# Kernel optimization log

Hardware: AMD Instinct MI355X
Metric: run time of the kernel (lower is better)

The kernel has to match this reference:

```python
import jax, jax.numpy as jnp
import numpy as np

M, K, N, R = 8192, 4096, 4096, 64  # tokens, in_features, out_features, pod_rank


def _unpack_int4(packed):
    """Unpack bytes (stored as int32 in [0,256)) into signed int4 values in [-8,7].
    Low nibble is element 2k, high nibble is element 2k+1."""
    b = packed.astype(jnp.int32)
    low = ((b & 0xF) ^ 8) - 8
    high = (((b >> 4) & 0xF) ^ 8) - 8
    out = jnp.stack([low, high], axis=-1)
    return out.reshape(packed.shape[:-1] + (packed.shape[-1] * 2,))


def setup_inputs() -> dict:
    key = jax.random.key(0)
    ks = jax.random.split(key, 7)
    x_quant = jax.random.randint(ks[0], (M, K // 2), 0, 256, dtype=jnp.int32)
    x_scale = jax.random.uniform(ks[1], (M,), dtype=jnp.float32) * 0.01 + 1e-4
    weight = jax.random.randint(ks[2], (N, K // 2), 0, 256, dtype=jnp.int32)
    weight_scales = jax.random.uniform(ks[3], (N, 1), dtype=jnp.float32) * 0.01 + 1e-4
    bias = jax.random.normal(ks[4], (N,), dtype=jnp.float32) * 0.02
    x_r = jax.random.normal(ks[5], (M, R), dtype=jnp.float32)
    w_outlier = jax.random.normal(ks[6], (N, R), dtype=jnp.float32) * 0.02
    return {"x_quant": x_quant, "x_scale": x_scale, "weight": weight,
            "weight_scales": weight_scales, "bias": bias, "x_r": x_r,
            "w_outlier": w_outlier}


def reference(x_quant, x_scale, weight, weight_scales, bias, x_r, w_outlier):
    xi = _unpack_int4(x_quant)          # [M, K] int32 in [-8,7]
    wi = _unpack_int4(weight)           # [N, K] int32 in [-8,7]
    y_int = jnp.matmul(xi, wi.T)        # [M, N] int32 accumulator
    # dequant: per-token activation scale * per-channel weight scale, plus bias
    y = (y_int.astype(jnp.float32) * x_scale[:, None] * weight_scales.reshape(1, -1)
         + bias[None, :])
    # fused low-rank outlier correction: addmm_(x_r, w_outlier.T)
    y = y + jnp.matmul(x_r, w_outlier.T)
    return y
```

## Files before the change

kernel.cpp:

```cpp
#include <hip/hip_runtime.h>
#include <hip/hip_fp16.h>

typedef int      v4i __attribute__((ext_vector_type(4)));
typedef int      v2i __attribute__((ext_vector_type(2)));
typedef float    v4f __attribute__((ext_vector_type(4)));
typedef _Float16 v8h __attribute__((ext_vector_type(8)));
typedef _Float16 v4h __attribute__((ext_vector_type(4)));

#define MDIM 8192
#define NDIM 4096
#define KDIM 4096
#define RDIM 64
#define KW   (KDIM / 2)
#define NT   (KDIM / 128)

typedef const __attribute__((address_space(1))) char* gas_ptr;
typedef __attribute__((address_space(3))) char*       las_ptr;

__device__ __forceinline__ void unpack_w(v4i w, int& lo8, int& hi8) {
    unsigned p01 = __builtin_amdgcn_perm((unsigned)w.y, (unsigned)w.x, 0x0C0C0400u);
    unsigned p23 = __builtin_amdgcn_perm((unsigned)w.w, (unsigned)w.z, 0x0C0C0400u);
    unsigned b4  = __builtin_amdgcn_perm(p23, p01, 0x05040100u);
    unsigned lo = b4 & 0x0F0F0F0Fu;
    unsigned hi = (b4 >> 4) & 0x0F0F0F0Fu;
    lo8 = (int)(((lo ^ 0x08080808u) + 0x78787878u) ^ 0x80808080u);
    hi8 = (int)(((hi ^ 0x08080808u) + 0x78787878u) ^ 0x80808080u);
}

__global__ __launch_bounds__(256)
void repack_int4(const int* __restrict__ xq, const int* __restrict__ wq,
                 char* __restrict__ x8, char* __restrict__ w8)
{
    const size_t XCH = (size_t)MDIM * KW / 4;
    const size_t TCH = XCH + (size_t)NDIM * KW / 4;
    size_t stride = (size_t)gridDim.x * blockDim.x;
    for (size_t i = (size_t)blockIdx.x * blockDim.x + threadIdx.x; i < TCH; i += stride) {
        const int* src;
        char* dst;
        if (i < XCH) { src = xq + i * 4; dst = x8 + i * 8; }
        else { size_t j = i - XCH; src = wq + j * 4; dst = w8 + j * 8; }
        v4i w = *(const v4i*)src;
        int lo8, hi8;
        unpack_w(w, lo8, hi8);
        *(v2i*)dst = (v2i){lo8, hi8};
    }
}

__device__ __forceinline__ void stage2(const char* g, char* l, int kt, int ks) {
    const char* s = g + kt * 128 + ks * 64;
    __builtin_amdgcn_global_load_lds((gas_ptr)(const void*)s,
                                     (las_ptr)(void*)l, 16, 0, 0);
    __builtin_amdgcn_global_load_lds((gas_ptr)(const void*)(s + (size_t)128 * KDIM),
                                     (las_ptr)(void*)(l + 8192), 16, 0, 0);
}

#define BAR asm volatile("s_barrier" ::: "memory")
#define VM4 asm volatile("s_waitcnt vmcnt(4)" ::: "memory")
#define SGB(m, n) __builtin_amdgcn_sched_group_barrier(m, n, 0)

#define SGBSEQ do {                                                            \
    SGB(0x100, 2); SGB(0x8, 4); SGB(0x100, 2); SGB(0x8, 4);                    \
    SGB(0x100, 2); SGB(0x8, 4); SGB(0x100, 2); SGB(0x8, 4);                    \
    SGB(0x100, 2); SGB(0x8, 4); SGB(0x100, 2); SGB(0x8, 4);                    \
    SGB(0x30, 2);  SGB(0x8, 4); SGB(0x30, 2);  SGB(0x8, 4);                    \
} while (0)

#define READ_A8(dst, PAR, KS)                                                  \
    _Pragma("unroll")                                                          \
    for (int ii = 0; ii < 8; ++ii)                                             \
        dst[ii] = *(const v4i*)((const char*)Asub[PAR][KS] + aoff + ii * 1024)

#define READ_B4(dst, PAR, KS)                                                  \
    _Pragma("unroll")                                                          \
    for (int jj = 0; jj < 4; ++jj)                                             \
        dst[jj] = *(const v4i*)((const char*)Bsub[PAR][KS] + boff + jj * 1024)

#define MMA32(AS, BS)                                                          \
    _Pragma("unroll")                                                          \
    for (int ii = 0; ii < 8; ++ii)                                             \
        _Pragma("unroll")                                                      \
        for (int jj = 0; jj < 4; ++jj)                                         \
            acc[ii][jj] = __builtin_amdgcn_mfma_i32_16x16x64_i8(               \
                AS[ii], BS[jj], acc[ii][jj], 0, 0, 0)

#define QPHASE(CA, CB, NA, NB, NPAR, NKS, SPAR, SKS, SKT) do {                 \
    READ_A8(NA, NPAR, NKS);                                                    \
    READ_B4(NB, NPAR, NKS);                                                    \
    stage2(gA, &Asub[SPAR][SKS][ldsW], SKT, SKS);                              \
    stage2(gB, &Bsub[SPAR][SKS][ldsW], SKT, SKS);                              \
    MMA32(CA, CB);                                                             \
    SGBSEQ;                                                                    \
    VM4; BAR;                                                                  \
} while (0)

__global__ __launch_bounds__(512, 2)
void w4a4_gemm8(const char* __restrict__ x8, const char* __restrict__ w8,
                const float* __restrict__ xsc, const float* __restrict__ wsc,
                const float* __restrict__ bias, const float* __restrict__ xr,
                const float* __restrict__ wo, float* __restrict__ out)
{
    __shared__ __align__(16) char Asub[2][2][16384];
    __shared__ __align__(16) char Bsub[2][2][16384];
    __shared__ float xs_s[256];
    __shared__ float ws_s[256];
    __shared__ float bs_s[256];

    const int tid  = threadIdx.x;
    const int lane = tid & 63;
    const int wid  = tid >> 6;
    const int wm   = wid >> 2;
    const int wn   = wid & 3;

    const int s  = (blockIdx.x & 7) * 64 + (blockIdx.x >> 3);
    const int by = s >> 4;
    const int bxn = s & 15;

    if (tid < 256) {
        xs_s[tid] = xsc[by * 256 + tid];
    } else {
        int n = tid - 256;
        ws_s[n] = wsc[bxn * 256 + n];
        bs_s[n] = bias[bxn * 256 + n];
    }

    const int srow = wid * 16 + (lane >> 2);
    const int scol = ((lane & 3) * 16) ^ (((lane >> 3) & 3) << 4);
    const char* gA = x8 + (size_t)(by * 256 + srow) * KDIM + scol;
    const char* gB = w8 + (size_t)(bxn * 256 + srow) * KDIM + scol;
    const int ldsW = wid * 1024;

    const int lr   = lane & 15;
    const int cef  = ((lane >> 4) << 4) ^ (((lr >> 1) & 3) << 4);
    const int aoff = (wm * 128 + lr) * 64 + cef;
    const int boff = (wn * 64  + lr) * 64 + cef;

    v4i acc[8][4];
#pragma unroll
    for (int i = 0; i < 8; ++i)
#pragma unroll
        for (int j = 0; j < 4; ++j) acc[i][j] = (v4i){0, 0, 0, 0};

    stage2(gA, &Asub[0][0][ldsW], 0, 0);
    stage2(gB, &Bsub[0][0][ldsW], 0, 0);
    stage2(gA, &Asub[0][1][ldsW], 0, 1);
    stage2(gB, &Bsub[0][1][ldsW], 0, 1);
    stage2(gA, &Asub[1][0][ldsW], 1, 0);
    stage2(gB, &Bsub[1][0][ldsW], 1, 0);
    VM4;
    BAR;

    v4i fa0[8], fb0[4], fa1[8], fb1[4];
    READ_A8(fa0, 0, 0);
    READ_B4(fb0, 0, 0);

    for (int it = 0; it < NT / 2; ++it) {
        const int kt1 = 2 * it + 1;
        const int kt2 = (2 * it + 2 < NT) ? 2 * it + 2 : NT - 1;
        const int kt3 = (2 * it + 3 < NT) ? 2 * it + 3 : NT - 1;
        QPHASE(fa0, fb0, fa1, fb1, 0, 1, 1, 1, kt1);
        QPHASE(fa1, fb1, fa0, fb0, 1, 0, 0, 0, kt2);
        QPHASE(fa0, fb0, fa1, fb1, 1, 1, 0, 1, kt2);
        QPHASE(fa1, fb1, fa0, fb0, 0, 0, 1, 0, kt3);
    }

    asm volatile("s_waitcnt vmcnt(0)" ::: "memory");
    BAR;

    _Float16* Xh = (_Float16*)&Asub[0][0][0];
    _Float16* Wh = (_Float16*)&Bsub[0][0][0];
    {
        const int rr = tid >> 3;
        const int c8 = (tid & 7) * 8;
#pragma unroll
        for (int p = 0; p < 4; ++p) {
            const int row = p * 64 + rr;
            v4f x0 = *(const v4f*)(xr + (size_t)(by * 256 + row) * RDIM + c8);
            v4f x1 = *(const v4f*)(xr + (size_t)(by * 256 + row) * RDIM + c8 + 4);
            v8h hx = {(_Float16)x0[0], (_Float16)x0[1], (_Float16)x0[2], (_Float16)x0[3],
                      (_Float16)x1[0], (_Float16)x1[1], (_Float16)x1[2], (_Float16)x1[3]};
            *(v8h*)((char*)Xh + (size_t)row * 144 + c8 * 2) = hx;
            v4f w0 = *(const v4f*)(wo + (size_t)(bxn * 256 + row) * RDIM + c8);
            v4f w1 = *(const v4f*)(wo + (size_t)(bxn * 256 + row) * RDIM + c8 + 4);
            v8h hw = {(_Float16)w0[0], (_Float16)w0[1], (_Float16)w0[2], (_Float16)w0[3],
                      (_Float16)w1[0], (_Float16)w1[1], (_Float16)w1[2], (_Float16)w1[3]};
            *(v8h*)((char*)Wh + (size_t)row * 144 + c8 * 2) = hw;
        }
    }

#pragma unroll
    for (int i = 0; i < 8; ++i) {
        const int r0 = wm * 128 + i * 16 + ((lane >> 4) << 2);
        const v4f xs4 = *(const v4f*)&xs_s[r0];
#pragma unroll
        for (int j = 0; j < 4; ++j) {
            const int col = wn * 64 + j * 16 + lr;
            const float sw = ws_s[col];
            const float bz = bs_s[col];
            v4f f;
#pragma unroll
            for (int r = 0; r < 4; ++r)
                f[r] = (float)acc[i][j][r] * xs4[r] * sw + bz;
            acc[i][j] = __builtin_bit_cast(v4i, f);
        }
    }
    __syncthreads();

#pragma unroll
    for (int ks = 0; ks < 2; ++ks) {
        v8h ah[8], bh[4];
#pragma unroll
        for (int i = 0; i < 8; ++i)
            ah[i] = *(const v8h*)((const char*)Xh +
                     (size_t)(wm * 128 + i * 16 + lr) * 144 + ks * 64 + ((lane >> 4) << 4));
#pragma unroll
        for (int j = 0; j < 4; ++j)
            bh[j] = *(const v8h*)((const char*)Wh +
                     (size_t)(wn * 64 + j * 16 + lr) * 144 + ks * 64 + ((lane >> 4) << 4));
#pragma unroll
        for (int i = 0; i < 8; ++i)
#pragma unroll
            for (int j = 0; j < 4; ++j) {
                v4f c = __builtin_bit_cast(v4f, acc[i][j]);
                c = __builtin_amdgcn_mfma_f32_16x16x32_f16(ah[i], bh[j], c, 0, 0, 0);
                acc[i][j] = __builtin_bit_cast(v4i, c);
            }
    }

    const size_t obase = (size_t)(by * 256 + wm * 128 + ((lane >> 4) << 2)) * NDIM
                       + bxn * 256 + wn * 64 + lr;
#pragma unroll
    for (int i = 0; i < 8; ++i)
#pragma unroll
        for (int j = 0; j < 4; ++j) {
            v4f f = __builtin_bit_cast(v4f, acc[i][j]);
#pragma unroll
            for (int r = 0; r < 4; ++r)
                out[obase + (size_t)(i * 16 + r) * NDIM + j * 16] = f[r];
        }
}

__global__ __launch_bounds__(256, 2)
void w4a4_fused(const int* __restrict__ xq, const float* __restrict__ xsc,
                const int* __restrict__ wq, const float* __restrict__ wsc,
                const float* __restrict__ bias, const float* __restrict__ xr,
                const float* __restrict__ wo, float* __restrict__ out)
{
    __shared__ __align__(16) char As[128 * 144];
    __shared__ __align__(16) char Bs[128 * 144];
    __shared__ float xs_s[128];
    __shared__ float ws_s[128];
    __shared__ float bs_s[128];

    const int tid  = threadIdx.x;
    const int lane = tid & 63;
    const int wid  = tid >> 6;
    const int wm   = wid >> 1;
    const int wn   = wid & 1;
    const int bx   = blockIdx.x % (NDIM / 128);
    const int by   = blockIdx.x / (NDIM / 128);

    const int srow   = tid >> 4;
    const int schunk = tid & 15;

    if (tid < 128) {
        xs_s[tid] = xsc[by * 128 + tid];
    } else {
        int n = tid - 128;
        ws_s[n] = wsc[bx * 128 + n];
        bs_s[n] = bias[bx * 128 + n];
    }

    const int* gA = xq + (size_t)(by * 128 + srow) * KW + schunk * 4;
    const int* gB = wq + (size_t)(bx * 128 + srow) * KW + schunk * 4;
    char* lA = As + srow * 144 + schunk * 8;
    char* lB = Bs + srow * 144 + schunk * 8;

    v4i acc[4][4];
#pragma unroll
    for (int i = 0; i < 4; ++i)
#pragma unroll
        for (int j = 0; j < 4; ++j) acc[i][j] = (v4i){0, 0, 0, 0};

    const int lr = lane & 15;
    const int lkb = (lane >> 4) * 16;

    for (int kt = 0; kt < KDIM / 128; ++kt) {
#pragma unroll
        for (int p = 0; p < 8; ++p) {
            v4i w = *(const v4i*)(gA + (size_t)p * 16 * KW + kt * 64);
            int lo8, hi8;
            unpack_w(w, lo8, hi8);
            *(v2i*)(lA + p * 16 * 144) = (v2i){lo8, hi8};
        }
#pragma unroll
        for (int p = 0; p < 8; ++p) {
            v4i w = *(const v4i*)(gB + (size_t)p * 16 * KW + kt * 64);
            int lo8, hi8;
            unpack_w(w, lo8, hi8);
            *(v2i*)(lB + p * 16 * 144) = (v2i){lo8, hi8};
        }
        __syncthreads();
#pragma unroll
        for (int ks = 0; ks < 2; ++ks) {
            v4i av[4], bv[4];
#pragma unroll
            for (int i = 0; i < 4; ++i)
                av[i] = *(const v4i*)(As + (wm * 64 + i * 16 + lr) * 144 + ks * 64 + lkb);
#pragma unroll
            for (int j = 0; j < 4; ++j)
                bv[j] = *(const v4i*)(Bs + (wn * 64 + j * 16 + lr) * 144 + ks * 64 + lkb);
#pragma unroll
            for (int i = 0; i < 4; ++i)
#pragma unroll
                for (int j = 0; j < 4; ++j)
                    acc[i][j] = __builtin_amdgcn_mfma_i32_16x16x64_i8(av[i], bv[j], acc[i][j], 0, 0, 0);
        }
        __syncthreads();
    }

    _Float16* Xh = (_Float16*)As;
    _Float16* Wh = (_Float16*)Bs;
#pragma unroll
    for (int p = 0; p < 8; ++p) {
        int row = p * 16 + srow;
        float4 vx = *(const float4*)(xr + (size_t)(by * 128 + row) * RDIM + schunk * 4);
        *(v4h*)(Xh + row * 72 + schunk * 4) =
            (v4h){(_Float16)vx.x, (_Float16)vx.y, (_Float16)vx.z, (_Float16)vx.w};
        float4 vw = *(const float4*)(wo + (size_t)(bx * 128 + row) * RDIM + schunk * 4);
        *(v4h*)(Wh + row * 72 + schunk * 4) =
            (v4h){(_Float16)vw.x, (_Float16)vw.y, (_Float16)vw.z, (_Float16)vw.w};
    }
    __syncthreads();

    v4f facc[4][4];
#pragma unroll
    for (int i = 0; i < 4; ++i)
#pragma unroll
        for (int j = 0; j < 4; ++j) facc[i][j] = (v4f){0.f, 0.f, 0.f, 0.f};

    const int lkh = (lane >> 4) * 8;
#pragma unroll
    for (int ks = 0; ks < 2; ++ks) {
        v8h ah[4], bh[4];
#pragma unroll
        for (int i = 0; i < 4; ++i)
            ah[i] = *(const v8h*)(Xh + (wm * 64 + i * 16 + lr) * 72 + ks * 32 + lkh);
#pragma unroll
        for (int j = 0; j < 4; ++j)
            bh[j] = *(const v8h*)(Wh + (wn * 64 + j * 16 + lr) * 72 + ks * 32 + lkh);
#pragma unroll
        for (int i = 0; i < 4; ++i)
#pragma unroll
            for (int j = 0; j < 4; ++j)
                facc[i][j] = __builtin_amdgcn_mfma_f32_16x16x32_f16(ah[i], bh[j], facc[i][j], 0, 0, 0);
    }

#pragma unroll
    for (int i = 0; i < 4; ++i) {
        int row0 = wm * 64 + i * 16 + (lane >> 4) * 4;
#pragma unroll
        for (int j = 0; j < 4; ++j) {
            int col = wn * 64 + j * 16 + lr;
            float sw = ws_s[col];
            float bz = bs_s[col];
#pragma unroll
            for (int r = 0; r < 4; ++r) {
                int row = row0 + r;
                float v = (float)acc[i][j][r] * xs_s[row] * sw + bz + facc[i][j][r];
                out[(size_t)(by * 128 + row) * NDIM + (bx * 128 + col)] = v;
            }
        }
    }
}

extern "C" void kernel_launch(void* const* d_in, const int* in_sizes, int n_in,
                              void* d_out, int out_size, void* d_ws, size_t ws_size,
                              hipStream_t stream) {
    const int*   xq   = (const int*)d_in[0];
    const float* xsc  = (const float*)d_in[1];
    const int*   wq   = (const int*)d_in[2];
    const float* wsc  = (const float*)d_in[3];
    const float* bias = (const float*)d_in[4];
    const float* xr   = (const float*)d_in[5];
    const float* wo   = (const float*)d_in[6];
    float* out = (float*)d_out;

    const size_t X8 = (size_t)MDIM * KDIM;
    const size_t W8 = (size_t)NDIM * KDIM;

    if (ws_size >= X8 + W8) {
        char* x8 = (char*)d_ws;
        char* w8 = x8 + X8;
        repack_int4<<<2048, 256, 0, stream>>>(xq, wq, x8, w8);
        w4a4_gemm8<<<(MDIM / 256) * (NDIM / 256), 512, 0, stream>>>(
            x8, w8, xsc, wsc, bias, xr, wo, out);
    } else {
        w4a4_fused<<<(MDIM / 128) * (NDIM / 128), 256, 0, stream>>>(
            xq, xsc, wq, wsc, bias, xr, wo, out);
    }
}
```

Measured before the change: 168.4 us.

## Switch int8 GEMM and low-rank epilogue to 32x32 MFMA tiles

Replaces the 16x16x64 int8 MFMA tiling with 32x32x32 int8 MFMAs, which changes the per-wave fragment layout to 4x2 tiles of 16-element accumulators. LDS fragment reads are reorganised to match. The low-rank epilogue now uses 32x32x16 f16 MFMAs over an XOR-swizzled 128-byte-row LDS layout in place of the padded 144-byte rows. The aim is fewer MFMA issues and fewer LDS fragment loads per k-step. In exchange the output scatter pattern and the swizzle need to be correct for the new 32x32 lane mapping.

After: 177.2 us. +5.3%, slower.

```diff
diff --git a/kernel.cpp b/kernel.cpp
--- a/kernel.cpp
+++ b/kernel.cpp
@@ -1,11 +1,13 @@
 #include <hip/hip_runtime.h>
 #include <hip/hip_fp16.h>
 
-typedef int      v4i __attribute__((ext_vector_type(4)));
-typedef int      v2i __attribute__((ext_vector_type(2)));
-typedef float    v4f __attribute__((ext_vector_type(4)));
-typedef _Float16 v8h __attribute__((ext_vector_type(8)));
-typedef _Float16 v4h __attribute__((ext_vector_type(4)));
+typedef int      v4i  __attribute__((ext_vector_type(4)));
+typedef int      v2i  __attribute__((ext_vector_type(2)));
+typedef int      v16i __attribute__((ext_vector_type(16)));
+typedef float    v4f  __attribute__((ext_vector_type(4)));
+typedef float    v16f __attribute__((ext_vector_type(16)));
+typedef _Float16 v8h  __attribute__((ext_vector_type(8)));
+typedef _Float16 v4h  __attribute__((ext_vector_type(4)));
 
 #define MDIM 8192
 #define NDIM 4096
@@ -59,45 +61,51 @@
 #define SGB(m, n) __builtin_amdgcn_sched_group_barrier(m, n, 0)
 
 #define SGBSEQ do {                                                            \
-    SGB(0x100, 2); SGB(0x8, 4); SGB(0x100, 2); SGB(0x8, 4);                    \
-    SGB(0x100, 2); SGB(0x8, 4); SGB(0x100, 2); SGB(0x8, 4);                    \
-    SGB(0x100, 2); SGB(0x8, 4); SGB(0x100, 2); SGB(0x8, 4);                    \
-    SGB(0x30, 2);  SGB(0x8, 4); SGB(0x30, 2);  SGB(0x8, 4);                    \
+    SGB(0x100, 2); SGB(0x8, 2); SGB(0x100, 2); SGB(0x8, 2);                    \
+    SGB(0x100, 2); SGB(0x8, 2); SGB(0x100, 2); SGB(0x8, 2);                    \
+    SGB(0x100, 2); SGB(0x8, 2); SGB(0x100, 2); SGB(0x8, 2);                    \
+    SGB(0x30, 2);  SGB(0x8, 2); SGB(0x30, 2);  SGB(0x8, 2);                    \
 } while (0)
 
-#define READ_A8(dst, PAR, KS)                                                  \
+#define READ_AB(DA, DB, PAR, KS_) do {                                         \
+    const char* Ab_ = (const char*)Asub[PAR][KS_];                             \
+    const char* Bb_ = (const char*)Bsub[PAR][KS_];                             \
     _Pragma("unroll")                                                          \
-    for (int ii = 0; ii < 8; ++ii)                                             \
-        dst[ii] = *(const v4i*)((const char*)Asub[PAR][KS] + aoff + ii * 1024)
-
-#define READ_B4(dst, PAR, KS)                                                  \
+    for (int ii = 0; ii < 4; ++ii) {                                           \
+        DA[ii][0] = *(const v4i*)(Ab_ + aoff + ii * 2048);                     \
+        DA[ii][1] = *(const v4i*)(Ab_ + (aoff ^ 32) + ii * 2048);              \
+    }                                                                          \
     _Pragma("unroll")                                                          \
-    for (int jj = 0; jj < 4; ++jj)                                             \
-        dst[jj] = *(const v4i*)((const char*)Bsub[PAR][KS] + boff + jj * 1024)
-
-#define MMA32(AS, BS)                                                          \
+    for (int jj = 0; jj < 2; ++jj) {                                           \
+        DB[jj][0] = *(const v4i*)(Bb_ + boff + jj * 2048);                     \
+        DB[jj][1] = *(const v4i*)(Bb_ + (boff ^ 32) + jj * 2048);              \
+    }                                                                          \
+} while (0)
+
+#define MMA16(AS, BS)                                                          \
     _Pragma("unroll")                                                          \
-    for (int ii = 0; ii < 8; ++ii)                                             \
+    for (int ks_ = 0; ks_ < 2; ++ks_)                                          \
         _Pragma("unroll")                                                      \
-        for (int jj = 0; jj < 4; ++jj)                                         \
-            acc[ii][jj] = __builtin_amdgcn_mfma_i32_16x16x64_i8(               \
-                AS[ii], BS[jj], acc[ii][jj], 0, 0, 0)
+        for (int ii = 0; ii < 4; ++ii)                                         \
+            _Pragma("unroll")                                                  \
+            for (int jj = 0; jj < 2; ++jj)                                     \
+                acc[ii][jj] = __builtin_amdgcn_mfma_i32_32x32x32_i8(           \
+                    AS[ii][ks_], BS[jj][ks_], acc[ii][jj], 0, 0, 0)
 
 #define QPHASE(CA, CB, NA, NB, NPAR, NKS, SPAR, SKS, SKT) do {                 \
-    READ_A8(NA, NPAR, NKS);                                                    \
-    READ_B4(NB, NPAR, NKS);                                                    \
+    READ_AB(NA, NB, NPAR, NKS);                                                \
     stage2(gA, &Asub[SPAR][SKS][ldsW], SKT, SKS);                              \
     stage2(gB, &Bsub[SPAR][SKS][ldsW], SKT, SKS);                              \
-    MMA32(CA, CB);                                                             \
+    MMA16(CA, CB);                                                             \
     SGBSEQ;                                                                    \
     VM4; BAR;                                                                  \
 } while (0)
 
 __global__ __launch_bounds__(512, 2)
-void w4a4_gemm8(const char* __restrict__ x8, const char* __restrict__ w8,
-                const float* __restrict__ xsc, const float* __restrict__ wsc,
-                const float* __restrict__ bias, const float* __restrict__ xr,
-                const float* __restrict__ wo, float* __restrict__ out)
+void w4a4_g32(const char* __restrict__ x8, const char* __restrict__ w8,
+              const float* __restrict__ xsc, const float* __restrict__ wsc,
+              const float* __restrict__ bias, const float* __restrict__ xr,
+              const float* __restrict__ wo, float* __restrict__ out)
 {
     __shared__ __align__(16) char Asub[2][2][16384];
     __shared__ __align__(16) char Bsub[2][2][16384];
@@ -129,16 +137,19 @@
     const char* gB = w8 + (size_t)(bxn * 256 + srow) * KDIM + scol;
     const int ldsW = wid * 1024;
 
-    const int lr   = lane & 15;
-    const int cef  = ((lane >> 4) << 4) ^ (((lr >> 1) & 3) << 4);
-    const int aoff = (wm * 128 + lr) * 64 + cef;
-    const int boff = (wn * 64  + lr) * 64 + cef;
-
-    v4i acc[8][4];
-#pragma unroll
-    for (int i = 0; i < 8; ++i)
-#pragma unroll
-        for (int j = 0; j < 4; ++j) acc[i][j] = (v4i){0, 0, 0, 0};
+    const int l31 = lane & 31;
+    const int kh  = lane >> 5;
+    const int cks = (kh << 4) ^ (((l31 >> 1) & 3) << 4);
+    const int aoff = (wm * 128 + l31) * 64 + cks;
+    const int boff = (wn * 64  + l31) * 64 + cks;
+
+    v16i acc[4][2];
+#pragma unroll
+    for (int i = 0; i < 4; ++i)
+#pragma unroll
+        for (int j = 0; j < 2; ++j)
+#pragma unroll
+            for (int r = 0; r < 16; ++r) acc[i][j][r] = 0;
 
     stage2(gA, &Asub[0][0][ldsW], 0, 0);
     stage2(gB, &Bsub[0][0][ldsW], 0, 0);
@@ -149,93 +160,104 @@
     VM4;
     BAR;
 
-    v4i fa0[8], fb0[4], fa1[8], fb1[4];
-    READ_A8(fa0, 0, 0);
-    READ_B4(fb0, 0, 0);
+    v4i a0[4][2], b0[2][2], a1[4][2], b1[2][2];
+    READ_AB(a0, b0, 0, 0);
 
     for (int it = 0; it < NT / 2; ++it) {
         const int kt1 = 2 * it + 1;
         const int kt2 = (2 * it + 2 < NT) ? 2 * it + 2 : NT - 1;
         const int kt3 = (2 * it + 3 < NT) ? 2 * it + 3 : NT - 1;
-        QPHASE(fa0, fb0, fa1, fb1, 0, 1, 1, 1, kt1);
-        QPHASE(fa1, fb1, fa0, fb0, 1, 0, 0, 0, kt2);
-        QPHASE(fa0, fb0, fa1, fb1, 1, 1, 0, 1, kt2);
-        QPHASE(fa1, fb1, fa0, fb0, 0, 0, 1, 0, kt3);
+        QPHASE(a0, b0, a1, b1, 0, 1, 1, 1, kt1);
+        QPHASE(a1, b1, a0, b0, 1, 0, 0, 0, kt2);
+        QPHASE(a0, b0, a1, b1, 1, 1, 0, 1, kt2);
+        QPHASE(a1, b1, a0, b0, 0, 0, 1, 0, kt3);
     }
 
     asm volatile("s_waitcnt vmcnt(0)" ::: "memory");
     BAR;
 
-    _Float16* Xh = (_Float16*)&Asub[0][0][0];
-    _Float16* Wh = (_Float16*)&Bsub[0][0][0];
+    char* Xh = (char*)&Asub[0][0][0];
+    char* Wh = (char*)&Bsub[0][0][0];
     {
         const int rr = tid >> 3;
-        const int c8 = (tid & 7) * 8;
+        const int cb = (tid & 7) * 16;
 #pragma unroll
         for (int p = 0; p < 4; ++p) {
             const int row = p * 64 + rr;
-            v4f x0 = *(const v4f*)(xr + (size_t)(by * 256 + row) * RDIM + c8);
-            v4f x1 = *(const v4f*)(xr + (size_t)(by * 256 + row) * RDIM + c8 + 4);
+            const int sw = cb ^ ((row & 7) << 4);
+            v4f x0 = *(const v4f*)(xr + (size_t)(by * 256 + row) * RDIM + (cb >> 1));
+            v4f x1 = *(const v4f*)(xr + (size_t)(by * 256 + row) * RDIM + (cb >> 1) + 4);
             v8h hx = {(_Float16)x0[0], (_Float16)x0[1], (_Float16)x0[2], (_Float16)x0[3],
                       (_Float16)x1[0], (_Float16)x1[1], (_Float16)x1[2], (_Float16)x1[3]};
-            *(v8h*)((char*)Xh + (size_t)row * 144 + c8 * 2) = hx;
-            v4f w0 = *(const v4f*)(wo + (size_t)(bxn * 256 + row) * RDIM + c8);
-            v4f w1 = *(const v4f*)(wo + (size_t)(bxn * 256 + row) * RDIM + c8 + 4);
+            *(v8h*)(Xh + (size_t)row * 128 + sw) = hx;
+            v4f w0 = *(const v4f*)(wo + (size_t)(bxn * 256 + row) * RDIM + (cb >> 1));
+            v4f w1 = *(const v4f*)(wo + (size_t)(bxn * 256 + row) * RDIM + (cb >> 1) + 4);
             v8h hw = {(_Float16)w0[0], (_Float16)w0[1], (_Float16)w0[2], (_Float16)w0[3],
                       (_Float16)w1[0], (_Float16)w1[1], (_Float16)w1[2], (_Float16)w1[3]};
-            *(v8h*)((char*)Wh + (size_t)row * 144 + c8 * 2) = hw;
-        }
-    }
-
-#pragma unroll
-    for (int i = 0; i < 8; ++i) {
-        const int r0 = wm * 128 + i * 16 + ((lane >> 4) << 2);
-        const v4f xs4 = *(const v4f*)&xs_s[r0];
-#pragma unroll
-        for (int j = 0; j < 4; ++j) {
-            const int col = wn * 64 + j * 16 + lr;
+            *(v8h*)(Wh + (size_t)row * 128 + sw) = hw;
+        }
+    }
+
+#pragma unroll
+    for (int i = 0; i < 4; ++i) {
+        const int r0 = wm * 128 + i * 32 + kh * 4;
+#pragma unroll
+        for (int j = 0; j < 2; ++j) {
+            const int col = wn * 64 + j * 32 + l31;
             const float sw = ws_s[col];
             const float bz = bs_s[col];
-            v4f f;
-#pragma unroll
-            for (int r = 0; r < 4; ++r)
-                f[r] = (float)acc[i][j][r] * xs4[r] * sw + bz;
-            acc[i][j] = __builtin_bit_cast(v4i, f);
+            v16f f;
+#pragma unroll
+            for (int q = 0; q < 4; ++q) {
+                const v4f xs4 = *(const v4f*)&xs_s[r0 + q * 8];
+#pragma unroll
+                for (int r = 0; r < 4; ++r)
+                    f[q * 4 + r] = (float)acc[i][j][q * 4 + r] * xs4[r] * sw + bz;
+            }
+            acc[i][j] = __builtin_bit_cast(v16i, f);
         }
     }
     __syncthreads();
 
-#pragma unroll
-    for (int ks = 0; ks < 2; ++ks) {
-        v8h ah[8], bh[4];
-#pragma unroll
-        for (int i = 0; i < 8; ++i)
-            ah[i] = *(const v8h*)((const char*)Xh +
-                     (size_t)(wm * 128 + i * 16 + lr) * 144 + ks * 64 + ((lane >> 4) << 4));
-#pragma unroll
-        for (int j = 0; j < 4; ++j)
-            bh[j] = *(const v8h*)((const char*)Wh +
-                     (size_t)(wn * 64 + j * 16 + lr) * 144 + ks * 64 + ((lane >> 4) << 4));
-#pragma unroll
-        for (int i = 0; i < 8; ++i)
-#pragma unroll
-            for (int j = 0; j < 4; ++j) {
-                v4f c = __builtin_bit_cast(v4f, acc[i][j]);
-                c = __builtin_amdgcn_mfma_f32_16x16x32_f16(ah[i], bh[j], c, 0, 0, 0);
-                acc[i][j] = __builtin_bit_cast(v4i, c);
+    const int obsw = (kh << 4) ^ ((l31 & 7) << 4);
+#pragma unroll
+    for (int ks = 0; ks < 4; ++ks) {
+        v8h ah[4], bh[2];
+#pragma unroll
+        for (int i = 0; i < 4; ++i) {
+            const int row = wm * 128 + i * 32 + l31;
+            ah[i] = *(const v8h*)(Xh + (size_t)row * 128 + (obsw ^ (ks << 5)));
+        }
+#pragma unroll
+        for (int j = 0; j < 2; ++j) {
+            const int row = wn * 64 + j * 32 + l31;
+            bh[j] = *(const v8h*)(Wh + (size_t)row * 128 + (obsw ^ (ks << 5)));
+        }
+#pragma unroll
+        for (int i = 0; i < 4; ++i)
+#pragma unroll
+            for (int j = 0; j < 2; ++j) {
+                v16f c = __builtin_bit_cast(v16f, acc[i][j]);
+                c = __builtin_amdgcn_mfma_f32_32x32x16_f16(ah[i], bh[j], c, 0, 0, 0);
+                acc[i][j] = __builtin_bit_cast(v16i, c);
             }
     }
 
-    const size_t obase = (size_t)(by * 256 + wm * 128 + ((lane >> 4) << 2)) * NDIM
-                       + bxn * 256 + wn * 64 + lr;
-#pragma unroll
-    for (int i = 0; i < 8; ++i)
-#pragma unroll
-        for (int j = 0; j < 4; ++j) {
-            v4f f = __builtin_bit_cast(v4f, acc[i][j]);
-#pragma unroll
-            for (int r = 0; r < 4; ++r)
-                out[obase + (size_t)(i * 16 + r) * NDIM + j * 16] = f[r];
+    const int colb = bxn * 256 + wn * 64 + l31;
+    const int rowb = by * 256 + wm * 128 + kh * 4;
+#pragma unroll
+    for (int i = 0; i < 4; ++i)
+#pragma unroll
+        for (int j = 0; j < 2; ++j) {
+            v16f f = __builtin_bit_cast(v16f, acc[i][j]);
+            const int col = colb + j * 32;
+#pragma unroll
+            for (int q = 0; q < 4; ++q) {
+                const int row = rowb + i * 32 + q * 8;
+#pragma unroll
+                for (int r = 0; r < 4; ++r)
+                    out[(size_t)(row + r) * NDIM + col] = f[q * 4 + r];
+            }
         }
 }
 
@@ -392,7 +414,7 @@
         char* x8 = (char*)d_ws;
         char* w8 = x8 + X8;
         repack_int4<<<2048, 256, 0, stream>>>(xq, wq, x8, w8);
-        w4a4_gemm8<<<(MDIM / 256) * (NDIM / 256), 512, 0, stream>>>(
+        w4a4_g32<<<(MDIM / 256) * (NDIM / 256), 512, 0, stream>>>(
             x8, w8, xsc, wsc, bias, xr, wo, out);
     } else {
         w4a4_fused<<<(MDIM / 128) * (NDIM / 128), 256, 0, stream>>>(
```
